# Performance work log

Hardware: AMD Instinct MI355X
Metric: run time of the kernel (lower is better)

Reference implementation:

```python
import jax, jax.numpy as jnp
import numpy as np

N_HEAD = 16
N_KV = 4
HEAD_DIM = 64
QK_SCALE = 1.2
VE_GATE_CH = 12


def rms_norm(x):
    # F.rms_norm with default eps = finfo(dtype).eps, no learned scale
    eps = jnp.asarray(jnp.finfo(x.dtype).eps, x.dtype)
    return x * jax.lax.rsqrt(jnp.mean(x * x, axis=-1, keepdims=True) + eps)


def apply_rotary(x, cos, sin):
    # x: (B,T,H,D); cos/sin: (1,T,1,D//2)
    d = x.shape[-1] // 2
    x1, x2 = x[..., :d], x[..., d:]
    return jnp.concatenate([x1 * cos + x2 * sin, -x1 * sin + x2 * cos], axis=-1)


def setup_inputs() -> dict:
    key = jax.random.key(0)
    ks = jax.random.split(key, 8)
    B, T, C = 2, 2048, 1024
    x = jax.random.normal(ks[0], (B, T, C), jnp.float32)
    ve = jax.random.normal(ks[1], (B, T, N_KV * HEAD_DIM), jnp.float32)
    # realistic rotary tables for positions 0..T
    half = HEAD_DIM // 2
    inv_freq = 1.0 / (10000.0 ** (np.arange(half, dtype=np.float64) / half))
    ang = np.arange(T)[:, None] * inv_freq[None, :]
    cos = jnp.asarray(np.cos(ang), jnp.float32)[None, :, None, :]
    sin = jnp.asarray(np.sin(ang), jnp.float32)[None, :, None, :]
    s = 0.02
    Wq = jax.random.normal(ks[2], (N_HEAD * HEAD_DIM, C), jnp.float32) * s
    Wk = jax.random.normal(ks[3], (N_KV * HEAD_DIM, C), jnp.float32) * s
    Wv = jax.random.normal(ks[4], (N_KV * HEAD_DIM, C), jnp.float32) * s
    Wo = jax.random.normal(ks[5], (C, C), jnp.float32) * s
    Wg = jax.random.normal(ks[6], (N_KV, VE_GATE_CH), jnp.float32) * s
    return dict(x=x, ve=ve, cos=cos, sin=sin, Wq=Wq, Wk=Wk, Wv=Wv, Wo=Wo,
                Wg=Wg, window_left=1024)


def reference(x, ve, cos, sin, Wq, Wk, Wv, Wo, Wg, window_left):
    B, T, C = x.shape
    G = N_HEAD // N_KV  # GQA group size
    q = (x @ Wq.T).reshape(B, T, N_HEAD, HEAD_DIM)
    k = (x @ Wk.T).reshape(B, T, N_KV, HEAD_DIM)
    v = (x @ Wv.T).reshape(B, T, N_KV, HEAD_DIM)
    # sigmoid-gated value-embedding mixing
    gate = 3.0 * jax.nn.sigmoid(x[..., :VE_GATE_CH] @ Wg.T)  # (B,T,N_KV)
    v = v + gate[..., None] * ve.reshape(B, T, N_KV, HEAD_DIM)
    # RoPE -> RMSNorm -> qk_scale on both q and k
    q = rms_norm(apply_rotary(q, cos, sin)) * QK_SCALE
    k = rms_norm(apply_rotary(k, cos, sin)) * QK_SCALE
    # GQA attention with causal + sliding window (flash default scale 1/sqrt(d))
    qg = q.reshape(B, T, N_KV, G, HEAD_DIM)
    scale = 1.0 / jnp.sqrt(jnp.asarray(HEAD_DIM, q.dtype))
    scores = jnp.einsum('bqkgd,bskd->bkgqs', qg, k) * scale  # (B,N_KV,G,T,T)
    i = jnp.arange(T)[:, None]
    j = jnp.arange(T)[None, :]
    mask = (j <= i) & (i - j <= window_left)
    scores = jnp.where(mask, scores, jnp.asarray(-1e30, scores.dtype))
    attn = jax.nn.softmax(scores, axis=-1)
    y = jnp.einsum('bkgqs,bskd->bqkgd', attn, v).reshape(B, T, N_HEAD * HEAD_DIM)
    return y @ Wo.T
```

## Files before the change

### kernel.cpp

```cpp
#include <hip/hip_runtime.h>
#include <hip/hip_bf16.h>

#define B_ 2
#define T_ 2048
#define C_ 1024
#define NH 16
#define NKV 4
#define HD 64
#define NQKV 1536
#define KVB 64

typedef __attribute__((ext_vector_type(4))) float f32x4;
typedef __attribute__((ext_vector_type(8))) short bf16x8;
typedef __attribute__((ext_vector_type(4))) short bf16x4;

__device__ __forceinline__ unsigned short f2bf(float f) {
  __hip_bfloat16 h = __float2bfloat16(f);
  unsigned short u;
  __builtin_memcpy(&u, &h, 2);
  return u;
}

__device__ __forceinline__ void gload16(const void* g, void* l) {
  __builtin_amdgcn_global_load_lds(
      (const __attribute__((address_space(1))) void*)g,
      (__attribute__((address_space(3))) void*)l, 16, 0, 0);
}

__device__ __forceinline__ unsigned cvtpk(float lo, float hi_) {
  unsigned w;
  asm("v_cvt_pk_bf16_f32 %0, %1, %2" : "=v"(w) : "v"(lo), "v"(hi_));
  return w;
}

#define NX4  1048576
#define NW4  262144
#define NK4  65536
#define O1 (NX4)
#define O2 (O1 + NW4)
#define O3 (O2 + NK4)
#define O4 (O3 + NK4)
#define OT (O4 + NW4)

__global__ __launch_bounds__(256) void conv_all(
    const float* __restrict__ x, const float* __restrict__ wq, const float* __restrict__ wk,
    const float* __restrict__ wv, const float* __restrict__ wo,
    unsigned short* __restrict__ xb, unsigned short* __restrict__ wqkvb,
    unsigned short* __restrict__ wob) {
  int i = blockIdx.x * blockDim.x + threadIdx.x;
  const int stride = gridDim.x * blockDim.x;
  for (; i < OT; i += stride) {
    const float* src;
    unsigned short* dst;
    int j;
    if (i < O1)      { src = x;  dst = xb;                    j = i; }
    else if (i < O2) { src = wq; dst = wqkvb;                 j = i - O1; }
    else if (i < O3) { src = wk; dst = wqkvb + 1024 * 1024;   j = i - O2; }
    else if (i < O4) { src = wv; dst = wqkvb + 1280 * 1024;   j = i - O3; }
    else             { src = wo; dst = wob;                   j = i - O4; }
    const float4 v = reinterpret_cast<const float4*>(src)[j];
    ushort4 o;
    o.x = f2bf(v.x); o.y = f2bf(v.y); o.z = f2bf(v.z); o.w = f2bf(v.w);
    reinterpret_cast<ushort4*>(dst)[j] = o;
  }
}

#define BK 64

__global__ __launch_bounds__(256) void gemm_qkv(
    const unsigned short* __restrict__ A, const unsigned short* __restrict__ Bw,
    const float* __restrict__ x, const float* __restrict__ ve,
    const float* __restrict__ cosb, const float* __restrict__ sinb,
    const float* __restrict__ Wg,
    unsigned short* __restrict__ Qn, unsigned short* __restrict__ Kn,
    unsigned short* __restrict__ Vt) {
  constexpr int BMT = 128, BNT = 64, MI = 4, NI = 2, K = 1024;
  __shared__ char smem[50176];
  unsigned short* AlB = (unsigned short*)smem;
  unsigned short* BlB = (unsigned short*)(smem + 32768);
  const int tid = threadIdx.x;
  const int lane = tid & 63;
  const int wid = tid >> 6;
  const int r = lane & 15, g = lane >> 4;
  const int wm = (wid >> 1) * 64, wn = (wid & 1) * 32;
  const int bm0 = blockIdx.y * BMT, bn0 = blockIdx.x * BNT;
  const int lrow = lane >> 3;
  const int lcol = ((lane & 7) ^ lrow) * 8;
  const unsigned short* Asrc = A + (size_t)(bm0 + wid * 32 + lrow) * K + lcol;
  const unsigned short* Bsrc = Bw + (size_t)(bn0 + wid * 16 + lrow) * K + lcol;
  const int fsw = (r & 7) << 4;
  f32x4 acc[MI][NI] = {};

  auto stage = [&](int k0, int buf) {
#pragma unroll
    for (int i = 0; i < 4; ++i)
      gload16(Asrc + (size_t)(i * 8) * K + k0, AlB + buf * 8192 + (wid * 32 + i * 8) * BK);
#pragma unroll
    for (int i = 0; i < 2; ++i)
      gload16(Bsrc + (size_t)(i * 8) * K + k0, BlB + buf * 4096 + (wid * 16 + i * 8) * BK);
  };

  stage(0, 0);
  __syncthreads();
  const int nt = K / BK;
  for (int t = 0; t < nt; ++t) {
    const int cur = t & 1;
    if (t + 1 < nt) stage((t + 1) * BK, cur ^ 1);
    const char* Ac = (const char*)(AlB + cur * 8192);
    const char* Bc = (const char*)(BlB + cur * 4096);
    bf16x8 af[MI][2], bfr[NI][2];
#pragma unroll
    for (int mi = 0; mi < MI; ++mi)
#pragma unroll
      for (int s = 0; s < 2; ++s)
        af[mi][s] = *reinterpret_cast<const bf16x8*>(
            Ac + (wm + mi * 16 + r) * 128 + ((s * 64 + g * 16) ^ fsw));
#pragma unroll
    for (int ni = 0; ni < NI; ++ni)
#pragma unroll
      for (int s = 0; s < 2; ++s)
        bfr[ni][s] = *reinterpret_cast<const bf16x8*>(
            Bc + (wn + ni * 16 + r) * 128 + ((s * 64 + g * 16) ^ fsw));
#pragma unroll
    for (int s = 0; s < 2; ++s)
#pragma unroll
      for (int mi = 0; mi < MI; ++mi)
#pragma unroll
        for (int ni = 0; ni < NI; ++ni)
          acc[mi][ni] = __builtin_amdgcn_mfma_f32_16x16x32_bf16(af[mi][s], bfr[ni][s],
                                                                acc[mi][ni], 0, 0, 0);
    __syncthreads();
  }
  float* Cl = (float*)smem;
  unsigned short* Vst = (unsigned short*)(smem + 33280);
#pragma unroll
  for (int mi = 0; mi < MI; ++mi)
#pragma unroll
    for (int ni = 0; ni < NI; ++ni)
#pragma unroll
      for (int e = 0; e < 4; ++e)
        Cl[(wm + mi * 16 + g * 4 + e) * 65 + wn + ni * 16 + r] = acc[mi][ni][e];
  __syncthreads();
  const int head = blockIdx.x;
  const int trow = tid >> 1, half = tid & 1;
  const int tg = bm0 + trow;
  const int b = tg >> 11, t = tg & 2047;
  if (head < 20) {
    float r1[16], r2[16];
    float sq = 0.f;
#pragma unroll
    for (int i = 0; i < 16; ++i) {
      const int d = half * 16 + i;
      const float x1 = Cl[trow * 65 + d];
      const float x2 = Cl[trow * 65 + d + 32];
      const float c = cosb[t * 32 + d];
      const float s = sinb[t * 32 + d];
      r1[i] = x1 * c + x2 * s;
      r2[i] = x2 * c - x1 * s;
      sq += r1[i] * r1[i] + r2[i] * r2[i];
    }
    sq += __shfl_xor(sq, 1);
    const float sc = rsqrtf(sq * (1.0f / 64.0f) + 1.1920929e-7f) *
                     ((head < 16) ? 0.21640425613334453f : 1.2f);
    unsigned short* dst = (head < 16)
        ? Qn + (((size_t)b * NH + head) * T_ + t) * HD
        : Kn + (((size_t)b * NKV + (head - 16)) * T_ + t) * HD;
#pragma unroll
    for (int i4 = 0; i4 < 4; ++i4) {
      ushort4 w1, w2;
      w1.x = f2bf(r1[i4 * 4 + 0] * sc); w1.y = f2bf(r1[i4 * 4 + 1] * sc);
      w1.z = f2bf(r1[i4 * 4 + 2] * sc); w1.w = f2bf(r1[i4 * 4 + 3] * sc);
      w2.x = f2bf(r2[i4 * 4 + 0] * sc); w2.y = f2bf(r2[i4 * 4 + 1] * sc);
      w2.z = f2bf(r2[i4 * 4 + 2] * sc); w2.w = f2bf(r2[i4 * 4 + 3] * sc);
      *reinterpret_cast<ushort4*>(dst + half * 16 + i4 * 4) = w1;
      *reinterpret_cast<ushort4*>(dst + half * 16 + 32 + i4 * 4) = w2;
    }
  } else {
    const int kv = head - 20;
    float dot = 0.f;
#pragma unroll
    for (int i = 0; i < 12; ++i) dot += x[(size_t)tg * C_ + i] * Wg[kv * 12 + i];
    const float gate = 3.0f / (1.0f + __expf(-dot));
    const float* vsrc = ve + (size_t)tg * (NKV * HD) + kv * HD;
#pragma unroll
    for (int i = 0; i < 32; ++i) {
      const int d = half * 32 + i;
      Vst[d * 128 + trow] = f2bf(Cl[trow * 65 + d] + gate * vsrc[d]);
    }
    __syncthreads();
    const int dd = tid >> 2, t0 = (tid & 3) * 32;
    unsigned short* vd = Vt + (((size_t)b * NKV + kv) * HD + dd) * T_ + (bm0 & 2047) + t0;
    const unsigned short* vs2 = Vst + dd * 128 + t0;
#pragma unroll
    for (int i = 0; i < 4; ++i)
      *reinterpret_cast<bf16x8*>(vd + i * 8) = *reinterpret_cast<const bf16x8*>(vs2 + i * 8);
  }
}

template <int BMT, int BNT, bool OUTBF>
__global__ __launch_bounds__(256) void gemm_bt(const unsigned short* __restrict__ A,
                                               const unsigned short* __restrict__ Bw,
                                               void* __restrict__ Cv, int M, int N, int K) {
  constexpr int MI = BMT / 32;
  constexpr int NI = BNT / 32;
  __shared__ unsigned short Al[2][BMT * BK];
  __shared__ unsigned short Bl[2][BNT * BK];
  const int tid = threadIdx.x;
  const int lane = tid & 63;
  const int wid = tid >> 6;
  const int r = lane & 15, g = lane >> 4;
  const int wm = (wid >> 1) * (BMT / 2), wn = (wid & 1) * (BNT / 2);
  const int bm0 = blockIdx.y * BMT, bn0 = blockIdx.x * BNT;
  const int lrow = lane >> 3;
  const int lcol = ((lane & 7) ^ lrow) * 8;
  const unsigned short* Asrc = A + (size_t)(bm0 + wid * (BMT / 4) + lrow) * K + lcol;
  const unsigned short* Bsrc = Bw + (size_t)(bn0 + wid * (BNT / 4) + lrow) * K + lcol;
  const int fsw = (r & 7) << 4;
  f32x4 acc[MI][NI] = {};

  auto stage = [&](int k0, int buf) {
#pragma unroll
    for (int i = 0; i < BMT / 32; ++i)
      gload16(Asrc + (size_t)(i * 8) * K + k0, Al[buf] + (wid * (BMT / 4) + i * 8) * BK);
#pragma unroll
    for (int i = 0; i < BNT / 32; ++i)
      gload16(Bsrc + (size_t)(i * 8) * K + k0, Bl[buf] + (wid * (BNT / 4) + i * 8) * BK);
  };

  stage(0, 0);
  __syncthreads();
  const int nt = K / BK;
  for (int t = 0; t < nt; ++t) {
    const int cur = t & 1;
    if (t + 1 < nt) stage((t + 1) * BK, cur ^ 1);
    const char* Ac = (const char*)Al[cur];
    const char* Bc = (const char*)Bl[cur];
    bf16x8 af[MI][2], bfr[NI][2];
#pragma unroll
    for (int mi = 0; mi < MI; ++mi)
#pragma unroll
      for (int s = 0; s < 2; ++s)
        af[mi][s] = *reinterpret_cast<const bf16x8*>(
            Ac + (wm + mi * 16 + r) * 128 + ((s * 64 + g * 16) ^ fsw));
#pragma unroll
    for (int ni = 0; ni < NI; ++ni)
#pragma unroll
      for (int s = 0; s < 2; ++s)
        bfr[ni][s] = *reinterpret_cast<const bf16x8*>(
            Bc + (wn + ni * 16 + r) * 128 + ((s * 64 + g * 16) ^ fsw));
#pragma unroll
    for (int s = 0; s < 2; ++s)
#pragma unroll
      for (int mi = 0; mi < MI; ++mi)
#pragma unroll
        for (int ni = 0; ni < NI; ++ni)
          acc[mi][ni] = __builtin_amdgcn_mfma_f32_16x16x32_bf16(af[mi][s], bfr[ni][s],
                                                                acc[mi][ni], 0, 0, 0);
    __syncthreads();
  }
#pragma unroll
  for (int mi = 0; mi < MI; ++mi)
#pragma unroll
    for (int ni = 0; ni < NI; ++ni) {
      const int row = bm0 + wm + mi * 16 + g * 4;
      const int col = bn0 + wn + ni * 16 + r;
#pragma unroll
      for (int e = 0; e < 4; ++e) {
        if (OUTBF)
          ((unsigned short*)Cv)[(size_t)(row + e) * N + col] = f2bf(acc[mi][ni][e]);
        else
          ((float*)Cv)[(size_t)(row + e) * N + col] = acc[mi][ni][e];
      }
    }
}

__global__ __launch_bounds__(256, 4) void attn_fwd(
    const unsigned short* __restrict__ Qn, const unsigned short* __restrict__ Kn,
    const unsigned short* __restrict__ Vt, unsigned short* __restrict__ Y,
    const int* __restrict__ wlp) {
  __shared__ unsigned short Kl[2][KVB * 64];
  __shared__ unsigned short Vl[2][64 * KVB];
  __shared__ unsigned short Pl[4][16 * 64];
  const int j = blockIdx.x, h = blockIdx.y, b = blockIdx.z;
  const int kvh = h >> 2;
  const int tid = threadIdx.x;
  const int wid = tid >> 6, lane = tid & 63;
  const int r = lane & 15, g = lane >> 4;
  const int wl = *wlp;
  const unsigned short* Kb = Kn + (size_t)(b * NKV + kvh) * T_ * HD;
  const unsigned short* Vb = Vt + (size_t)(b * NKV + kvh) * HD * T_;
  const int srow = tid >> 3;
  const int scolb = (tid & 7) * 16;
  const int sdst = srow * 128 + (scolb ^ ((srow & 7) << 4));
  const unsigned short* Ksrc0 = Kb + (size_t)srow * HD + (scolb >> 1);
  const unsigned short* Ksrc1 = Kb + (size_t)(srow + 32) * HD + (scolb >> 1);
  const unsigned short* Vsrc0 = Vb + (size_t)srow * T_ + (scolb >> 1);
  const unsigned short* Vsrc1 = Vb + (size_t)(srow + 32) * T_ + (scolb >> 1);
  char* Pwb = (char*)Pl[wid];
  const int swz = (r & 7) << 4;
  const int ksw = swz;
  const int nseg = (j < 8) ? 2 : 1;

  for (int seg = 0; seg < nseg; ++seg) {
    const int qt = (j < 8) ? (seg ? 15 - j : j) : j + 8;
    const int q0 = qt * 64;
    const int qs = q0 + wid * 16;
    const int q = qs + r;
    const unsigned short* Qb = Qn + ((size_t)(b * NH + h) * T_ + qs) * HD;
    const bf16x8 qf0 = *reinterpret_cast<const bf16x8*>(Qb + r * HD + g * 8);
    const bf16x8 qf1 = *reinterpret_cast<const bf16x8*>(Qb + r * HD + 32 + g * 8);
    float lrun = 0.f;
    f32x4 o[4] = {};
    int slo = q0 - wl; if (slo < 0) slo = 0;
    slo &= ~63;
    const int send = q0 + 63;

    bf16x8 ska, skb, sva, svb;
    ska = *reinterpret_cast<const bf16x8*>(Ksrc0 + (size_t)slo * HD);
    skb = *reinterpret_cast<const bf16x8*>(Ksrc1 + (size_t)slo * HD);
    sva = *reinterpret_cast<const bf16x8*>(Vsrc0 + slo);
    svb = *reinterpret_cast<const bf16x8*>(Vsrc1 + slo);
    {
      char* Kd = (char*)Kl[0]; char* Vd = (char*)Vl[0];
      *reinterpret_cast<bf16x8*>(Kd + sdst) = ska;
      *reinterpret_cast<bf16x8*>(Kd + 32 * 128 + sdst) = skb;
      *reinterpret_cast<bf16x8*>(Vd + sdst) = sva;
      *reinterpret_cast<bf16x8*>(Vd + 32 * 128 + sdst) = svb;
    }
    __syncthreads();

    int cur = 0;
    for (int sb = slo; sb <= send; sb += KVB) {
      const bool has_next = (sb + KVB <= send);
      if (has_next) {
        const int nb = sb + KVB;
        ska = *reinterpret_cast<const bf16x8*>(Ksrc0 + (size_t)nb * HD);
        skb = *reinterpret_cast<const bf16x8*>(Ksrc1 + (size_t)nb * HD);
        sva = *reinterpret_cast<const bf16x8*>(Vsrc0 + nb);
        svb = *reinterpret_cast<const bf16x8*>(Vsrc1 + nb);
      }
      {
        const char* Kc = (const char*)Kl[cur];
        const char* Vc = (const char*)Vl[cur];
        float sv[16];
        __builtin_amdgcn_s_setprio(1);
#pragma unroll
        for (int sub = 0; sub < 4; ++sub) {
          const int rowb = (sub * 16 + r) * 128;
          bf16x8 kf0 = *reinterpret_cast<const bf16x8*>(Kc + rowb + ((g * 16) ^ ksw));
          bf16x8 kf1 = *reinterpret_cast<const bf16x8*>(Kc + rowb + ((64 + g * 16) ^ ksw));
          f32x4 z = {};
          z = __builtin_amdgcn_mfma_f32_16x16x32_bf16(kf0, qf0, z, 0, 0, 0);
          z = __builtin_amdgcn_mfma_f32_16x16x32_bf16(kf1, qf1, z, 0, 0, 0);
#pragma unroll
          for (int e = 0; e < 4; ++e) sv[sub * 4 + e] = z[e];
        }
        __builtin_amdgcn_s_setprio(0);
        if (sb + 63 > qs || sb < qs + 15 - wl) {
#pragma unroll
          for (int i = 0; i < 16; ++i) {
            const int s_ = sb + (i >> 2) * 16 + g * 4 + (i & 3);
            const bool ok = (unsigned)(q - s_) <= (unsigned)wl;
            sv[i] = ok ? sv[i] : -__builtin_inff();
          }
        }
        float pe[16];
        float ps = 0.f;
#pragma unroll
        for (int i = 0; i < 16; ++i) {
          pe[i] = exp2f(sv[i] - 17.0f);
          ps += pe[i];
        }
        lrun += ps;
#pragma unroll
        for (int sub = 0; sub < 4; ++sub) {
          unsigned w2[2];
          w2[0] = cvtpk(pe[sub * 4 + 0], pe[sub * 4 + 1]);
          w2[1] = cvtpk(pe[sub * 4 + 2], pe[sub * 4 + 3]);
          bf16x4 w;
          __builtin_memcpy(&w, w2, 8);
          *reinterpret_cast<bf16x4*>(Pwb + ((r * 128 + sub * 32 + g * 8) ^ swz)) = w;
        }
        asm volatile("s_waitcnt lgkmcnt(0)" ::: "memory");
        __builtin_amdgcn_s_setprio(1);
#pragma unroll
        for (int c = 0; c < 2; ++c) {
          const bf16x8 pf = *reinterpret_cast<const bf16x8*>(Pwb + ((r * 128 + c * 64 + g * 16) ^ swz));
#pragma unroll
          for (int dt = 0; dt < 4; ++dt) {
            const int vrow = (dt * 16 + r) * 128;
            const bf16x8 vf = *reinterpret_cast<const bf16x8*>(Vc + vrow + ((c * 64 + g * 16) ^ ksw));
            o[dt] = __builtin_amdgcn_mfma_f32_16x16x32_bf16(vf, pf, o[dt], 0, 0, 0);
          }
        }
        __builtin_amdgcn_s_setprio(0);
      }
      if (has_next) {
        char* Kd = (char*)Kl[cur ^ 1]; char* Vd = (char*)Vl[cur ^ 1];
        *reinterpret_cast<bf16x8*>(Kd + sdst) = ska;
        *reinterpret_cast<bf16x8*>(Kd + 32 * 128 + sdst) = skb;
        *reinterpret_cast<bf16x8*>(Vd + sdst) = sva;
        *reinterpret_cast<bf16x8*>(Vd + 32 * 128 + sdst) = svb;
      }
      __syncthreads();
      cur ^= 1;
    }
    lrun += __shfl_xor(lrun, 16);
    lrun += __shfl_xor(lrun, 32);
    const float inv = 1.0f / lrun;
    unsigned short* Yb = Y + ((size_t)(b * T_) + qs + r) * (NH * HD) + h * HD;
#pragma unroll
    for (int dt = 0; dt < 4; ++dt)
#pragma unroll
      for (int e = 0; e < 4; ++e)
        Yb[dt * 16 + g * 4 + e] = f2bf(o[dt][e] * inv);
  }
}

extern "C" void kernel_launch(void* const* d_in, const int* in_sizes, int n_in,
                              void* d_out, int out_size, void* d_ws, size_t ws_size,
                              hipStream_t stream) {
  const float* x    = (const float*)d_in[0];
  const float* ve   = (const float*)d_in[1];
  const float* cosb = (const float*)d_in[2];
  const float* sinb = (const float*)d_in[3];
  const float* Wq   = (const float*)d_in[4];
  const float* Wk   = (const float*)d_in[5];
  const float* Wv   = (const float*)d_in[6];
  const float* Wo   = (const float*)d_in[7];
  const float* Wg   = (const float*)d_in[8];
  const int*   wlp  = (const int*)d_in[9];

  char* ws = (char*)d_ws;
  unsigned short* xb    = (unsigned short*)ws; ws += (size_t)4096 * 1024 * 2;
  unsigned short* wqkvb = (unsigned short*)ws; ws += (size_t)1536 * 1024 * 2;
  unsigned short* wob   = (unsigned short*)ws; ws += (size_t)1024 * 1024 * 2;
  unsigned short* Qn    = (unsigned short*)ws; ws += (size_t)B_ * NH * T_ * HD * 2;
  unsigned short* Kn    = (unsigned short*)ws; ws += (size_t)B_ * NKV * T_ * HD * 2;
  unsigned short* Vt    = (unsigned short*)ws; ws += (size_t)B_ * NKV * HD * T_ * 2;
  unsigned short* yb    = (unsigned short*)ws; ws += (size_t)4096 * 1024 * 2;

  conv_all<<<dim3(2048), dim3(256), 0, stream>>>(x, Wq, Wk, Wv, Wo, xb, wqkvb, wob);

  gemm_qkv<<<dim3(NQKV / 64, 4096 / 128), dim3(256), 0, stream>>>(
      xb, wqkvb, x, ve, cosb, sinb, Wg, Qn, Kn, Vt);

  attn_fwd<<<dim3(24, NH, B_), dim3(256), 0, stream>>>(Qn, Kn, Vt, yb, wlp);

  gemm_bt<128, 64, false><<<dim3(1024 / 64, 4096 / 128), dim3(256), 0, stream>>>(
      yb, wob, d_out, 4096, 1024, 1024);
}
```

Baseline: 81.20 us.

## Deepen attention KV prefetch to two tiles and remap grid for KV-head locality

The attention kernel now keeps two register sets of K/V prefetch in flight, so the global load for tile i+2 is issued before computing tile i. The loop is unrolled by two with explicit buffers and lighter asm barriers. The grid is flattened to 1D so that consecutive blocks share a KV head and batch, which should improve L2 reuse of K/V across the four query heads of a group. This costs extra registers for the second prefetch set, which may lower occupancy.

```diff
diff --git a/kernel.cpp b/kernel.cpp
--- a/kernel.cpp
+++ b/kernel.cpp
@@ -74,7 +74,7 @@
     const float* __restrict__ Wg,
     unsigned short* __restrict__ Qn, unsigned short* __restrict__ Kn,
     unsigned short* __restrict__ Vt) {
-  constexpr int BMT = 128, BNT = 64, MI = 4, NI = 2, K = 1024;
+  constexpr int BMT = 128, MI = 4, NI = 2, K = 1024;
   __shared__ char smem[50176];
   unsigned short* AlB = (unsigned short*)smem;
   unsigned short* BlB = (unsigned short*)(smem + 32768);
@@ -83,7 +83,7 @@
   const int wid = tid >> 6;
   const int r = lane & 15, g = lane >> 4;
   const int wm = (wid >> 1) * 64, wn = (wid & 1) * 32;
-  const int bm0 = blockIdx.y * BMT, bn0 = blockIdx.x * BNT;
+  const int bm0 = blockIdx.y * BMT, bn0 = blockIdx.x * 64;
   const int lrow = lane >> 3;
   const int lcol = ((lane & 7) ^ lrow) * 8;
   const unsigned short* Asrc = A + (size_t)(bm0 + wid * 32 + lrow) * K + lcol;
@@ -281,8 +281,11 @@
   __shared__ unsigned short Kl[2][KVB * 64];
   __shared__ unsigned short Vl[2][64 * KVB];
   __shared__ unsigned short Pl[4][16 * 64];
-  const int j = blockIdx.x, h = blockIdx.y, b = blockIdx.z;
-  const int kvh = h >> 2;
+  const int flat = blockIdx.x;
+  const int kvh = flat & 3, b = (flat >> 2) & 1;
+  const int slot = flat >> 3;
+  const int h = kvh * 4 + (slot & 3);
+  const int j = slot >> 2;
   const int tid = threadIdx.x;
   const int wid = tid >> 6, lane = tid & 63;
   const int r = lane & 15, g = lane >> 4;
@@ -301,6 +304,23 @@
   const int ksw = swz;
   const int nseg = (j < 8) ? 2 : 1;
 
+#define LOADR(P, IDX)                                                            \
+  P##ka = *reinterpret_cast<const bf16x8*>(Ksrc0 + (size_t)(slo + (IDX) * 64) * HD); \
+  P##kb = *reinterpret_cast<const bf16x8*>(Ksrc1 + (size_t)(slo + (IDX) * 64) * HD); \
+  P##va = *reinterpret_cast<const bf16x8*>(Vsrc0 + slo + (IDX) * 64);                \
+  P##vb = *reinterpret_cast<const bf16x8*>(Vsrc1 + slo + (IDX) * 64);
+
+#define WRITES(P, BUF)                                                \
+  {                                                                   \
+    char* Kd = (char*)Kl[BUF]; char* Vd = (char*)Vl[BUF];             \
+    *reinterpret_cast<bf16x8*>(Kd + sdst) = P##ka;                    \
+    *reinterpret_cast<bf16x8*>(Kd + 32 * 128 + sdst) = P##kb;         \
+    *reinterpret_cast<bf16x8*>(Vd + sdst) = P##va;                    \
+    *reinterpret_cast<bf16x8*>(Vd + 32 * 128 + sdst) = P##vb;         \
+  }
+
+#define BARR() asm volatile("s_waitcnt lgkmcnt(0)\n\ts_barrier" ::: "memory")
+
   for (int seg = 0; seg < nseg; ++seg) {
     const int qt = (j < 8) ? (seg ? 15 - j : j) : j + 8;
     const int q0 = qt * 64;
@@ -313,97 +333,83 @@
     f32x4 o[4] = {};
     int slo = q0 - wl; if (slo < 0) slo = 0;
     slo &= ~63;
-    const int send = q0 + 63;
-
-    bf16x8 ska, skb, sva, svb;
-    ska = *reinterpret_cast<const bf16x8*>(Ksrc0 + (size_t)slo * HD);
-    skb = *reinterpret_cast<const bf16x8*>(Ksrc1 + (size_t)slo * HD);
-    sva = *reinterpret_cast<const bf16x8*>(Vsrc0 + slo);
-    svb = *reinterpret_cast<const bf16x8*>(Vsrc1 + slo);
-    {
-      char* Kd = (char*)Kl[0]; char* Vd = (char*)Vl[0];
-      *reinterpret_cast<bf16x8*>(Kd + sdst) = ska;
-      *reinterpret_cast<bf16x8*>(Kd + 32 * 128 + sdst) = skb;
-      *reinterpret_cast<bf16x8*>(Vd + sdst) = sva;
-      *reinterpret_cast<bf16x8*>(Vd + 32 * 128 + sdst) = svb;
-    }
+    const int nt = (q0 - slo) / 64 + 1;
+
+    auto comp = [&](int sb, int buf) {
+      const char* Kc = (const char*)Kl[buf];
+      const char* Vc = (const char*)Vl[buf];
+      float sv[16];
+      __builtin_amdgcn_s_setprio(1);
+#pragma unroll
+      for (int sub = 0; sub < 4; ++sub) {
+        const int rowb = (sub * 16 + r) * 128;
+        bf16x8 kf0 = *reinterpret_cast<const bf16x8*>(Kc + rowb + ((g * 16) ^ ksw));
+        bf16x8 kf1 = *reinterpret_cast<const bf16x8*>(Kc + rowb + ((64 + g * 16) ^ ksw));
+        f32x4 z = {};
+        z = __builtin_amdgcn_mfma_f32_16x16x32_bf16(kf0, qf0, z, 0, 0, 0);
+        z = __builtin_amdgcn_mfma_f32_16x16x32_bf16(kf1, qf1, z, 0, 0, 0);
+#pragma unroll
+        for (int e = 0; e < 4; ++e) sv[sub * 4 + e] = z[e];
+      }
+      __builtin_amdgcn_s_setprio(0);
+      if (sb + 63 > qs || sb < qs + 15 - wl) {
+#pragma unroll
+        for (int i = 0; i < 16; ++i) {
+          const int s_ = sb + (i >> 2) * 16 + g * 4 + (i & 3);
+          const bool ok = (unsigned)(q - s_) <= (unsigned)wl;
+          sv[i] = ok ? sv[i] : -__builtin_inff();
+        }
+      }
+      float pe[16];
+      float ps = 0.f;
+#pragma unroll
+      for (int i = 0; i < 16; ++i) {
+        pe[i] = exp2f(sv[i] - 17.0f);
+        ps += pe[i];
+      }
+      lrun += ps;
+#pragma unroll
+      for (int sub = 0; sub < 4; ++sub) {
+        unsigned w2[2];
+        w2[0] = cvtpk(pe[sub * 4 + 0], pe[sub * 4 + 1]);
+        w2[1] = cvtpk(pe[sub * 4 + 2], pe[sub * 4 + 3]);
+        bf16x4 w;
+        __builtin_memcpy(&w, w2, 8);
+        *reinterpret_cast<bf16x4*>(Pwb + ((r * 128 + sub * 32 + g * 8) ^ swz)) = w;
+      }
+      asm volatile("s_waitcnt lgkmcnt(0)" ::: "memory");
+      __builtin_amdgcn_s_setprio(1);
+#pragma unroll
+      for (int c = 0; c < 2; ++c) {
+        const bf16x8 pf = *reinterpret_cast<const bf16x8*>(Pwb + ((r * 128 + c * 64 + g * 16) ^ swz));
+#pragma unroll
+        for (int dt = 0; dt < 4; ++dt) {
+          const int vrow = (dt * 16 + r) * 128;
+          const bf16x8 vf = *reinterpret_cast<const bf16x8*>(Vc + vrow + ((c * 64 + g * 16) ^ ksw));
+          o[dt] = __builtin_amdgcn_mfma_f32_16x16x32_bf16(vf, pf, o[dt], 0, 0, 0);
+        }
+      }
+      __builtin_amdgcn_s_setprio(0);
+    };
+
+    bf16x8 Aka, Akb, Ava, Avb, Bka, Bkb, Bva, Bvb;
+    if (seg) __syncthreads();
+    LOADR(A, 0)
+    if (nt > 1) { LOADR(B, 1) }
+    WRITES(A, 0)
     __syncthreads();
 
-    int cur = 0;
-    for (int sb = slo; sb <= send; sb += KVB) {
-      const bool has_next = (sb + KVB <= send);
-      if (has_next) {
-        const int nb = sb + KVB;
-        ska = *reinterpret_cast<const bf16x8*>(Ksrc0 + (size_t)nb * HD);
-        skb = *reinterpret_cast<const bf16x8*>(Ksrc1 + (size_t)nb * HD);
-        sva = *reinterpret_cast<const bf16x8*>(Vsrc0 + nb);
-        svb = *reinterpret_cast<const bf16x8*>(Vsrc1 + nb);
-      }
-      {
-        const char* Kc = (const char*)Kl[cur];
-        const char* Vc = (const char*)Vl[cur];
-        float sv[16];
-        __builtin_amdgcn_s_setprio(1);
-#pragma unroll
-        for (int sub = 0; sub < 4; ++sub) {
-          const int rowb = (sub * 16 + r) * 128;
-          bf16x8 kf0 = *reinterpret_cast<const bf16x8*>(Kc + rowb + ((g * 16) ^ ksw));
-          bf16x8 kf1 = *reinterpret_cast<const bf16x8*>(Kc + rowb + ((64 + g * 16) ^ ksw));
-          f32x4 z = {};
-          z = __builtin_amdgcn_mfma_f32_16x16x32_bf16(kf0, qf0, z, 0, 0, 0);
-          z = __builtin_amdgcn_mfma_f32_16x16x32_bf16(kf1, qf1, z, 0, 0, 0);
-#pragma unroll
-          for (int e = 0; e < 4; ++e) sv[sub * 4 + e] = z[e];
-        }
-        __builtin_amdgcn_s_setprio(0);
-        if (sb + 63 > qs || sb < qs + 15 - wl) {
-#pragma unroll
-          for (int i = 0; i < 16; ++i) {
-            const int s_ = sb + (i >> 2) * 16 + g * 4 + (i & 3);
-            const bool ok = (unsigned)(q - s_) <= (unsigned)wl;
-            sv[i] = ok ? sv[i] : -__builtin_inff();
-          }
-        }
-        float pe[16];
-        float ps = 0.f;
-#pragma unroll
-        for (int i = 0; i < 16; ++i) {
-          pe[i] = exp2f(sv[i] - 17.0f);
-          ps += pe[i];
-        }
-        lrun += ps;
-#pragma unroll
-        for (int sub = 0; sub < 4; ++sub) {
-          unsigned w2[2];
-          w2[0] = cvtpk(pe[sub * 4 + 0], pe[sub * 4 + 1]);
-          w2[1] = cvtpk(pe[sub * 4 + 2], pe[sub * 4 + 3]);
-          bf16x4 w;
-          __builtin_memcpy(&w, w2, 8);
-          *reinterpret_cast<bf16x4*>(Pwb + ((r * 128 + sub * 32 + g * 8) ^ swz)) = w;
-        }
-        asm volatile("s_waitcnt lgkmcnt(0)" ::: "memory");
-        __builtin_amdgcn_s_setprio(1);
-#pragma unroll
-        for (int c = 0; c < 2; ++c) {
-          const bf16x8 pf = *reinterpret_cast<const bf16x8*>(Pwb + ((r * 128 + c * 64 + g * 16) ^ swz));
-#pragma unroll
-          for (int dt = 0; dt < 4; ++dt) {
-            const int vrow = (dt * 16 + r) * 128;
-            const bf16x8 vf = *reinterpret_cast<const bf16x8*>(Vc + vrow + ((c * 64 + g * 16) ^ ksw));
-            o[dt] = __builtin_amdgcn_mfma_f32_16x16x32_bf16(vf, pf, o[dt], 0, 0, 0);
-          }
-        }
-        __builtin_amdgcn_s_setprio(0);
-      }
-      if (has_next) {
-        char* Kd = (char*)Kl[cur ^ 1]; char* Vd = (char*)Vl[cur ^ 1];
-        *reinterpret_cast<bf16x8*>(Kd + sdst) = ska;
-        *reinterpret_cast<bf16x8*>(Kd + 32 * 128 + sdst) = skb;
-        *reinterpret_cast<bf16x8*>(Vd + sdst) = sva;
-        *reinterpret_cast<bf16x8*>(Vd + 32 * 128 + sdst) = svb;
-      }
-      __syncthreads();
-      cur ^= 1;
+    for (int i = 0; i < nt; i += 2) {
+      if (i + 2 < nt) { LOADR(A, i + 2) }
+      comp(slo + i * 64, 0);
+      if (i + 1 < nt) {
+        WRITES(B, 1)
+        BARR();
+        if (i + 3 < nt) { LOADR(B, i + 3) }
+        comp(slo + (i + 1) * 64, 1);
+        if (i + 2 < nt) { WRITES(A, 0) }
+        BARR();
+      }
     }
     lrun += __shfl_xor(lrun, 16);
     lrun += __shfl_xor(lrun, 32);
@@ -415,6 +421,9 @@
       for (int e = 0; e < 4; ++e)
         Yb[dt * 16 + g * 4 + e] = f2bf(o[dt][e] * inv);
   }
+#undef LOADR
+#undef WRITES
+#undef BARR
 }
 
 extern "C" void kernel_launch(void* const* d_in, const int* in_sizes, int n_in,
@@ -445,7 +454,7 @@
   gemm_qkv<<<dim3(NQKV / 64, 4096 / 128), dim3(256), 0, stream>>>(
       xb, wqkvb, x, ve, cosb, sinb, Wg, Qn, Kn, Vt);
 
-  attn_fwd<<<dim3(24, NH, B_), dim3(256), 0, stream>>>(Qn, Kn, Vt, yb, wlp);
+  attn_fwd<<<dim3(768), dim3(256), 0, stream>>>(Qn, Kn, Vt, yb, wlp);
 
   gemm_bt<128, 64, false><<<dim3(1024 / 64, 4096 / 128), dim3(256), 0, stream>>>(
       yb, wob, d_out, 4096, 1024, 1024);
```

Result: no change. 81.25 us (+0.1%).

## Load V fragments directly from global into registers, remap attention grid

Applied to the files above, without the earlier changes.

The attention kernel stops staging V tiles through LDS. Each lane now loads its V MFMA operands straight from global memory (the transposed Vt layout) into registers every iteration. The launch becomes a flat 1D grid ordered so that blocks sharing a KV head and batch sit next to each other, which should improve L2 reuse of K/V. It also switches exp2f to the hardware exp2 intrinsic. The aim is less LDS traffic and write/read work, at the cost of unprefetched global loads landing on the critical path each tile.

```diff
diff --git a/kernel.cpp b/kernel.cpp
--- a/kernel.cpp
+++ b/kernel.cpp
@@ -74,7 +74,7 @@
     const float* __restrict__ Wg,
     unsigned short* __restrict__ Qn, unsigned short* __restrict__ Kn,
     unsigned short* __restrict__ Vt) {
-  constexpr int BMT = 128, BNT = 64, MI = 4, NI = 2, K = 1024;
+  constexpr int BMT = 128, MI = 4, NI = 2, K = 1024;
   __shared__ char smem[50176];
   unsigned short* AlB = (unsigned short*)smem;
   unsigned short* BlB = (unsigned short*)(smem + 32768);
@@ -83,7 +83,7 @@
   const int wid = tid >> 6;
   const int r = lane & 15, g = lane >> 4;
   const int wm = (wid >> 1) * 64, wn = (wid & 1) * 32;
-  const int bm0 = blockIdx.y * BMT, bn0 = blockIdx.x * BNT;
+  const int bm0 = blockIdx.y * BMT, bn0 = blockIdx.x * 64;
   const int lrow = lane >> 3;
   const int lcol = ((lane & 7) ^ lrow) * 8;
   const unsigned short* Asrc = A + (size_t)(bm0 + wid * 32 + lrow) * K + lcol;
@@ -279,10 +279,12 @@
     const unsigned short* __restrict__ Vt, unsigned short* __restrict__ Y,
     const int* __restrict__ wlp) {
   __shared__ unsigned short Kl[2][KVB * 64];
-  __shared__ unsigned short Vl[2][64 * KVB];
   __shared__ unsigned short Pl[4][16 * 64];
-  const int j = blockIdx.x, h = blockIdx.y, b = blockIdx.z;
-  const int kvh = h >> 2;
+  const int flat = blockIdx.x;
+  const int kvh = flat & 3, b = (flat >> 2) & 1;
+  const int slot = flat >> 3;
+  const int h = kvh * 4 + (slot & 3);
+  const int j = slot >> 2;
   const int tid = threadIdx.x;
   const int wid = tid >> 6, lane = tid & 63;
   const int r = lane & 15, g = lane >> 4;
@@ -294,8 +296,10 @@
   const int sdst = srow * 128 + (scolb ^ ((srow & 7) << 4));
   const unsigned short* Ksrc0 = Kb + (size_t)srow * HD + (scolb >> 1);
   const unsigned short* Ksrc1 = Kb + (size_t)(srow + 32) * HD + (scolb >> 1);
-  const unsigned short* Vsrc0 = Vb + (size_t)srow * T_ + (scolb >> 1);
-  const unsigned short* Vsrc1 = Vb + (size_t)(srow + 32) * T_ + (scolb >> 1);
+  const unsigned short* Vr0 = Vb + (size_t)(0 * 16 + r) * T_ + g * 8;
+  const unsigned short* Vr1 = Vb + (size_t)(1 * 16 + r) * T_ + g * 8;
+  const unsigned short* Vr2 = Vb + (size_t)(2 * 16 + r) * T_ + g * 8;
+  const unsigned short* Vr3 = Vb + (size_t)(3 * 16 + r) * T_ + g * 8;
   char* Pwb = (char*)Pl[wid];
   const int swz = (r & 7) << 4;
   const int ksw = swz;
@@ -313,35 +317,35 @@
     f32x4 o[4] = {};
     int slo = q0 - wl; if (slo < 0) slo = 0;
     slo &= ~63;
-    const int send = q0 + 63;
-
-    bf16x8 ska, skb, sva, svb;
+    const int nt = (q0 - slo) / 64 + 1;
+
+    bf16x8 ska, skb;
     ska = *reinterpret_cast<const bf16x8*>(Ksrc0 + (size_t)slo * HD);
     skb = *reinterpret_cast<const bf16x8*>(Ksrc1 + (size_t)slo * HD);
-    sva = *reinterpret_cast<const bf16x8*>(Vsrc0 + slo);
-    svb = *reinterpret_cast<const bf16x8*>(Vsrc1 + slo);
     {
-      char* Kd = (char*)Kl[0]; char* Vd = (char*)Vl[0];
+      char* Kd = (char*)Kl[0];
       *reinterpret_cast<bf16x8*>(Kd + sdst) = ska;
       *reinterpret_cast<bf16x8*>(Kd + 32 * 128 + sdst) = skb;
-      *reinterpret_cast<bf16x8*>(Vd + sdst) = sva;
-      *reinterpret_cast<bf16x8*>(Vd + 32 * 128 + sdst) = svb;
     }
     __syncthreads();
 
     int cur = 0;
-    for (int sb = slo; sb <= send; sb += KVB) {
-      const bool has_next = (sb + KVB <= send);
-      if (has_next) {
-        const int nb = sb + KVB;
-        ska = *reinterpret_cast<const bf16x8*>(Ksrc0 + (size_t)nb * HD);
-        skb = *reinterpret_cast<const bf16x8*>(Ksrc1 + (size_t)nb * HD);
-        sva = *reinterpret_cast<const bf16x8*>(Vsrc0 + nb);
-        svb = *reinterpret_cast<const bf16x8*>(Vsrc1 + nb);
+    for (int i = 0; i < nt; ++i) {
+      const int sb = slo + i * 64;
+      if (i + 1 < nt) {
+        ska = *reinterpret_cast<const bf16x8*>(Ksrc0 + (size_t)(sb + 64) * HD);
+        skb = *reinterpret_cast<const bf16x8*>(Ksrc1 + (size_t)(sb + 64) * HD);
       }
+      bf16x8 vr0 = *reinterpret_cast<const bf16x8*>(Vr0 + sb);
+      bf16x8 vr1 = *reinterpret_cast<const bf16x8*>(Vr1 + sb);
+      bf16x8 vr2 = *reinterpret_cast<const bf16x8*>(Vr2 + sb);
+      bf16x8 vr3 = *reinterpret_cast<const bf16x8*>(Vr3 + sb);
+      bf16x8 vr4 = *reinterpret_cast<const bf16x8*>(Vr0 + sb + 32);
+      bf16x8 vr5 = *reinterpret_cast<const bf16x8*>(Vr1 + sb + 32);
+      bf16x8 vr6 = *reinterpret_cast<const bf16x8*>(Vr2 + sb + 32);
+      bf16x8 vr7 = *reinterpret_cast<const bf16x8*>(Vr3 + sb + 32);
       {
         const char* Kc = (const char*)Kl[cur];
-        const char* Vc = (const char*)Vl[cur];
         float sv[16];
         __builtin_amdgcn_s_setprio(1);
 #pragma unroll
@@ -358,18 +362,18 @@
         __builtin_amdgcn_s_setprio(0);
         if (sb + 63 > qs || sb < qs + 15 - wl) {
 #pragma unroll
-          for (int i = 0; i < 16; ++i) {
-            const int s_ = sb + (i >> 2) * 16 + g * 4 + (i & 3);
+          for (int i2 = 0; i2 < 16; ++i2) {
+            const int s_ = sb + (i2 >> 2) * 16 + g * 4 + (i2 & 3);
             const bool ok = (unsigned)(q - s_) <= (unsigned)wl;
-            sv[i] = ok ? sv[i] : -__builtin_inff();
+            sv[i2] = ok ? sv[i2] : -__builtin_inff();
           }
         }
         float pe[16];
         float ps = 0.f;
 #pragma unroll
-        for (int i = 0; i < 16; ++i) {
-          pe[i] = exp2f(sv[i] - 17.0f);
-          ps += pe[i];
+        for (int i2 = 0; i2 < 16; ++i2) {
+          pe[i2] = __builtin_amdgcn_exp2f(sv[i2] - 17.0f);
+          ps += pe[i2];
         }
         lrun += ps;
 #pragma unroll
@@ -383,24 +387,24 @@
         }
         asm volatile("s_waitcnt lgkmcnt(0)" ::: "memory");
         __builtin_amdgcn_s_setprio(1);
-#pragma unroll
-        for (int c = 0; c < 2; ++c) {
-          const bf16x8 pf = *reinterpret_cast<const bf16x8*>(Pwb + ((r * 128 + c * 64 + g * 16) ^ swz));
-#pragma unroll
-          for (int dt = 0; dt < 4; ++dt) {
-            const int vrow = (dt * 16 + r) * 128;
-            const bf16x8 vf = *reinterpret_cast<const bf16x8*>(Vc + vrow + ((c * 64 + g * 16) ^ ksw));
-            o[dt] = __builtin_amdgcn_mfma_f32_16x16x32_bf16(vf, pf, o[dt], 0, 0, 0);
-          }
+        {
+          const bf16x8 pf0 = *reinterpret_cast<const bf16x8*>(Pwb + ((r * 128 + g * 16) ^ swz));
+          o[0] = __builtin_amdgcn_mfma_f32_16x16x32_bf16(vr0, pf0, o[0], 0, 0, 0);
+          o[1] = __builtin_amdgcn_mfma_f32_16x16x32_bf16(vr1, pf0, o[1], 0, 0, 0);
+          o[2] = __builtin_amdgcn_mfma_f32_16x16x32_bf16(vr2, pf0, o[2], 0, 0, 0);
+          o[3] = __builtin_amdgcn_mfma_f32_16x16x32_bf16(vr3, pf0, o[3], 0, 0, 0);
+          const bf16x8 pf1 = *reinterpret_cast<const bf16x8*>(Pwb + ((r * 128 + 64 + g * 16) ^ swz));
+          o[0] = __builtin_amdgcn_mfma_f32_16x16x32_bf16(vr4, pf1, o[0], 0, 0, 0);
+          o[1] = __builtin_amdgcn_mfma_f32_16x16x32_bf16(vr5, pf1, o[1], 0, 0, 0);
+          o[2] = __builtin_amdgcn_mfma_f32_16x16x32_bf16(vr6, pf1, o[2], 0, 0, 0);
+          o[3] = __builtin_amdgcn_mfma_f32_16x16x32_bf16(vr7, pf1, o[3], 0, 0, 0);
         }
         __builtin_amdgcn_s_setprio(0);
       }
-      if (has_next) {
-        char* Kd = (char*)Kl[cur ^ 1]; char* Vd = (char*)Vl[cur ^ 1];
+      if (i + 1 < nt) {
+        char* Kd = (char*)Kl[cur ^ 1];
         *reinterpret_cast<bf16x8*>(Kd + sdst) = ska;
         *reinterpret_cast<bf16x8*>(Kd + 32 * 128 + sdst) = skb;
-        *reinterpret_cast<bf16x8*>(Vd + sdst) = sva;
-        *reinterpret_cast<bf16x8*>(Vd + 32 * 128 + sdst) = svb;
       }
       __syncthreads();
       cur ^= 1;
@@ -445,7 +449,7 @@
   gemm_qkv<<<dim3(NQKV / 64, 4096 / 128), dim3(256), 0, stream>>>(
       xb, wqkvb, x, ve, cosb, sinb, Wg, Qn, Kn, Vt);
 
-  attn_fwd<<<dim3(24, NH, B_), dim3(256), 0, stream>>>(Qn, Kn, Vt, yb, wlp);
+  attn_fwd<<<dim3(768), dim3(256), 0, stream>>>(Qn, Kn, Vt, yb, wlp);
 
   gemm_bt<128, 64, false><<<dim3(1024 / 64, 4096 / 128), dim3(256), 0, stream>>>(
       yb, wob, d_out, 4096, 1024, 1024);
```

Result: slower. 104.0 us (+28.1%).
